# Optimization experiments

Hardware: AMD Instinct MI355X
Metric: run time of the kernel (lower is better)

The kernel has to match this reference:

```python
import jax, jax.numpy as jnp
import numpy as np

NUM_NODES = 10000
NODE_DIM = 128
EDGE_DIM = 128
HIDDEN_DIM = 128
OUT_DIM = 128
N_EDGES = 640000


def setup_inputs() -> dict:
    key = jax.random.key(0)
    k = jax.random.split(key, 8)
    x = jax.random.normal(k[0], (NUM_NODES, NODE_DIM), dtype=jnp.float32)
    edge_index = jax.random.randint(k[1], (2, N_EDGES), 0, NUM_NODES, dtype=jnp.int64)
    edge_attr = jax.random.normal(k[2], (N_EDGES, EDGE_DIM), dtype=jnp.float32)
    # node2edge linear: in = 2*node_dim + edge_dim
    s1 = 1.0 / np.sqrt(2 * NODE_DIM + EDGE_DIM)
    W1 = jax.random.uniform(k[3], (2 * NODE_DIM + EDGE_DIM, HIDDEN_DIM), jnp.float32, -s1, s1)
    b1 = jax.random.uniform(k[4], (HIDDEN_DIM,), jnp.float32, -s1, s1)
    # edge2node linear: in = hidden_dim + node_dim
    s2 = 1.0 / np.sqrt(HIDDEN_DIM + NODE_DIM)
    W2 = jax.random.uniform(k[5], (HIDDEN_DIM + NODE_DIM, OUT_DIM), jnp.float32, -s2, s2)
    b2 = jax.random.uniform(k[6], (OUT_DIM,), jnp.float32, -s2, s2)
    return {"x": x, "edge_index": edge_index, "edge_attr": edge_attr,
            "W1": W1, "b1": b1, "W2": W2, "b2": b2}


def reference(x, edge_index, edge_attr, W1, b1, W2, b2):
    src, dst = edge_index[0], edge_index[1]
    # Node2Edge: gather endpoints, concat with edge features, linear
    h_i = x[src]                                   # [E, node_dim]
    h_j = x[dst]                                   # [E, node_dim]
    inp_e = jnp.concatenate([h_i, h_j, edge_attr], axis=-1)  # [E, 2*nd+ed]
    h_edge = inp_e @ W1 + b1                       # [E, hidden]
    # Edge2Node: scatter-sum edge embeddings to target nodes (edge_index[1])
    agg = jax.ops.segment_sum(h_edge, dst, num_segments=NUM_NODES)  # [N, hidden]
    inp_n = jnp.concatenate([agg, x], axis=-1)     # [N, hidden+nd]
    h_node = inp_n @ W2 + b2                       # [N, out]
    return h_node
```

## Files before the change

kernel.cpp:

```cpp
#include <hip/hip_runtime.h>


#define NN 10000
#define ED 640000
#define D  128

typedef __bf16 bf16;
typedef bf16  bf16x8 __attribute__((ext_vector_type(8)));
typedef float f32x4  __attribute__((ext_vector_type(4)));

__device__ __forceinline__ bf16 f2b(float f) {
  unsigned u = __builtin_bit_cast(unsigned, f);
  u += 0x7fffu + ((u >> 16) & 1u);
  unsigned short h = (unsigned short)(u >> 16);
  return __builtin_bit_cast(bf16, h);
}

__device__ __forceinline__ bf16x8 bzero8() {
  bf16 z = __builtin_bit_cast(bf16, (unsigned short)0);
  bf16x8 v = {z, z, z, z, z, z, z, z};
  return v;
}

__global__ __launch_bounds__(256) void k_prep(const float* __restrict__ x,
                                              const float* __restrict__ W1,
                                              const float* __restrict__ W2,
                                              bf16* __restrict__ xb,
                                              bf16* __restrict__ W1p,
                                              bf16* __restrict__ W2p,
                                              int* __restrict__ counts) {
  int id = blockIdx.x * 256 + threadIdx.x;
  if (id < 160000) {
    int i = id * 8;
    f32x4 a = *(const f32x4*)(x + i);
    f32x4 b = *(const f32x4*)(x + i + 4);
    bf16x8 h;
    h[0]=f2b(a[0]); h[1]=f2b(a[1]); h[2]=f2b(a[2]); h[3]=f2b(a[3]);
    h[4]=f2b(b[0]); h[5]=f2b(b[1]); h[6]=f2b(b[2]); h[7]=f2b(b[3]);
    *(bf16x8*)(xb + i) = h;
  } else if (id < 170000) {
    counts[id - 160000] = 0;
  } else if (id < 176144) {
    int o8 = id - 170000;
    int kb = o8 >> 9, rem = o8 & 511, t = rem >> 6, L = rem & 63;
    int col  = t * 16 + (L & 15);
    int row0 = kb * 32 + (L >> 4) * 8;
    bf16x8 h;
    #pragma unroll
    for (int j = 0; j < 8; j++) h[j] = f2b(W1[(row0 + j) * D + col]);
    *(bf16x8*)(W1p + o8 * 8) = h;
  } else if (id < 180240) {
    int o8 = id - 176144;
    int kb = o8 >> 9, rem = o8 & 511, t = rem >> 6, L = rem & 63;
    int col  = t * 16 + (L & 15);
    int row0 = kb * 32 + (L >> 4) * 8;
    bf16x8 h;
    #pragma unroll
    for (int j = 0; j < 8; j++) h[j] = f2b(W2[(row0 + j) * D + col]);
    *(bf16x8*)(W2p + o8 * 8) = h;
  }
}

__global__ __launch_bounds__(256) void k_hist(const int* __restrict__ dst,
                                              int* __restrict__ counts) {
  int e = blockIdx.x * 256 + threadIdx.x;
  if (e < ED) atomicAdd(&counts[dst[e]], 1);
}

__global__ __launch_bounds__(256) void k_scan(const int* __restrict__ counts,
                                              int* __restrict__ row_ptr,
                                              int* __restrict__ fill_ptr) {
  __shared__ int part[256];
  int tid = threadIdx.x;
  const int CH = 40;
  int base = tid * CH;
  int sum = 0;
  for (int i = 0; i < CH; i++) { int idx = base + i; if (idx < NN) sum += counts[idx]; }
  part[tid] = sum;
  __syncthreads();
  for (int off = 1; off < 256; off <<= 1) {
    int v = (tid >= off) ? part[tid - off] : 0;
    __syncthreads();
    part[tid] += v;
    __syncthreads();
  }
  int run = part[tid] - sum;
  for (int i = 0; i < CH; i++) {
    int idx = base + i;
    if (idx < NN) { row_ptr[idx] = run; fill_ptr[idx] = run; run += counts[idx]; }
  }
  if (tid == 255) row_ptr[NN] = part[255];
}

__global__ __launch_bounds__(256) void k_fill(const int* __restrict__ src,
                                              const int* __restrict__ dst,
                                              int* __restrict__ fill_ptr,
                                              int2* __restrict__ csr) {
  int e = blockIdx.x * 256 + threadIdx.x;
  if (e < ED) {
    int d = dst[e];
    int pos = atomicAdd(&fill_ptr[d], 1);
    csr[pos] = make_int2(e, src[e]);
  }
}

__global__ __launch_bounds__(256) void k_sum(const bf16*  __restrict__ xb,
                                             const float* __restrict__ ea,
                                             const int*   __restrict__ row_ptr,
                                             const int2*  __restrict__ csr,
                                             float* __restrict__ sx,
                                             float* __restrict__ sea) {
  int gwave = (blockIdx.x * 256 + threadIdx.x) >> 6;
  if (gwave >= NN) return;
  int lane = threadIdx.x & 63;
  int g = lane >> 4, l = lane & 15;
  int e0 = row_ptr[gwave], e1 = row_ptr[gwave + 1];

  f32x4 ax0 = {0.f,0.f,0.f,0.f}, ax1 = {0.f,0.f,0.f,0.f};
  f32x4 ae0 = {0.f,0.f,0.f,0.f}, ae1 = {0.f,0.f,0.f,0.f};

  #pragma unroll 2
  for (int e = e0 + g; e < e1; e += 4) {
    int2 es = csr[e];
    bf16x8 hx = *(const bf16x8*)(xb + (size_t)es.y * D + l * 8);
    const float* ep = ea + (size_t)es.x * D + l * 8;
    f32x4 f0 = *(const f32x4*)ep;
    f32x4 f1 = *(const f32x4*)(ep + 4);
    ax0[0] += (float)hx[0]; ax0[1] += (float)hx[1];
    ax0[2] += (float)hx[2]; ax0[3] += (float)hx[3];
    ax1[0] += (float)hx[4]; ax1[1] += (float)hx[5];
    ax1[2] += (float)hx[6]; ax1[3] += (float)hx[7];
    ae0 += f0;
    ae1 += f1;
  }
  #pragma unroll
  for (int i = 0; i < 4; i++) {
    ax0[i] += __shfl_xor(ax0[i], 16, 64); ax0[i] += __shfl_xor(ax0[i], 32, 64);
    ax1[i] += __shfl_xor(ax1[i], 16, 64); ax1[i] += __shfl_xor(ax1[i], 32, 64);
    ae0[i] += __shfl_xor(ae0[i], 16, 64); ae0[i] += __shfl_xor(ae0[i], 32, 64);
    ae1[i] += __shfl_xor(ae1[i], 16, 64); ae1[i] += __shfl_xor(ae1[i], 32, 64);
  }
  if (lane < 16) {
    float* px = sx  + (size_t)gwave * D + l * 8;
    float* pe = sea + (size_t)gwave * D + l * 8;
    *(f32x4*)px       = ax0;
    *(f32x4*)(px + 4) = ax1;
    *(f32x4*)pe       = ae0;
    *(f32x4*)(pe + 4) = ae1;
  }
}

__global__ __launch_bounds__(256) void k_out(const float* __restrict__ sx,
                                             const float* __restrict__ sea,
                                             const bf16*  __restrict__ xb,
                                             const bf16*  __restrict__ W1p,
                                             const bf16*  __restrict__ W2p,
                                             const float* __restrict__ b1,
                                             const float* __restrict__ b2,
                                             const int*   __restrict__ row_ptr,
                                             float* __restrict__ out) {
  __shared__ __align__(16) bf16 lds[64 * 392];
  int tid  = threadIdx.x;
  int wave = tid >> 6, lane = tid & 63, quad = lane >> 4, l16 = lane & 15;
  int n0 = blockIdx.x * 64;

  #pragma unroll
  for (int i = 0; i < 4; i++) {
    int m = (tid >> 4) + 16 * i;
    int v = n0 + m;
    int cl = tid & 15;
    float cntf = (v < NN) ? (float)(row_ptr[v + 1] - row_ptr[v]) : 0.f;
    #pragma unroll
    for (int j = 0; j < 3; j++) {
      int c = cl + 16 * j;
      bf16x8 h;
      if (v < NN) {
        if (j == 0) {
          const float* p = sx + (size_t)v * D + cl * 8;
          f32x4 f0 = *(const f32x4*)p, f1 = *(const f32x4*)(p + 4);
          h[0]=f2b(f0[0]); h[1]=f2b(f0[1]); h[2]=f2b(f0[2]); h[3]=f2b(f0[3]);
          h[4]=f2b(f1[0]); h[5]=f2b(f1[1]); h[6]=f2b(f1[2]); h[7]=f2b(f1[3]);
        } else if (j == 1) {
          bf16x8 hx = *(const bf16x8*)(xb + (size_t)v * D + cl * 8);
          #pragma unroll
          for (int k = 0; k < 8; k++) h[k] = f2b((float)hx[k] * cntf);
        } else {
          const float* p = sea + (size_t)v * D + cl * 8;
          f32x4 f0 = *(const f32x4*)p, f1 = *(const f32x4*)(p + 4);
          h[0]=f2b(f0[0]); h[1]=f2b(f0[1]); h[2]=f2b(f0[2]); h[3]=f2b(f0[3]);
          h[4]=f2b(f1[0]); h[5]=f2b(f1[1]); h[6]=f2b(f1[2]); h[7]=f2b(f1[3]);
        }
      } else h = bzero8();
      *(bf16x8*)&lds[m * 392 + c * 8] = h;
    }
  }
  __syncthreads();

  f32x4 acc[4][2];
  #pragma unroll
  for (int mt = 0; mt < 4; mt++)
    #pragma unroll
    for (int tt = 0; tt < 2; tt++) acc[mt][tt] = (f32x4){0.f, 0.f, 0.f, 0.f};

  #pragma unroll
  for (int kb = 0; kb < 12; kb++) {
    bf16x8 B0 = *(const bf16x8*)(W1p + ((kb * 8 + wave * 2 + 0) * 64 + lane) * 8);
    bf16x8 B1 = *(const bf16x8*)(W1p + ((kb * 8 + wave * 2 + 1) * 64 + lane) * 8);
    #pragma unroll
    for (int mt = 0; mt < 4; mt++) {
      bf16x8 a = *(const bf16x8*)&lds[(mt * 16 + l16) * 392 + kb * 32 + quad * 8];
      acc[mt][0] = __builtin_amdgcn_mfma_f32_16x16x32_bf16(a, B0, acc[mt][0], 0, 0, 0);
      acc[mt][1] = __builtin_amdgcn_mfma_f32_16x16x32_bf16(a, B1, acc[mt][1], 0, 0, 0);
    }
  }
  __syncthreads();

  #pragma unroll
  for (int tt = 0; tt < 2; tt++) {
    int col = wave * 32 + tt * 16 + l16;
    float bb = b1[col];
    #pragma unroll
    for (int mt = 0; mt < 4; mt++)
      #pragma unroll
      for (int r = 0; r < 4; r++) {
        int m = mt * 16 + quad * 4 + r;
        int v = n0 + m;
        float cntf = (v < NN) ? (float)(row_ptr[v + 1] - row_ptr[v]) : 0.f;
        lds[m * 264 + col] = f2b(acc[mt][tt][r] + cntf * bb);
      }
  }
  #pragma unroll
  for (int i = 0; i < 4; i++) {
    int m = (tid >> 4) + 16 * i;
    int c = tid & 15;
    int v = n0 + m;
    bf16x8 h = (v < NN) ? *(const bf16x8*)(xb + (size_t)v * D + c * 8) : bzero8();
    *(bf16x8*)&lds[m * 264 + 128 + c * 8] = h;
  }
  __syncthreads();

  f32x4 acc2[4][2];
  #pragma unroll
  for (int mt = 0; mt < 4; mt++)
    #pragma unroll
    for (int tt = 0; tt < 2; tt++) acc2[mt][tt] = (f32x4){0.f, 0.f, 0.f, 0.f};

  #pragma unroll
  for (int kb = 0; kb < 8; kb++) {
    bf16x8 B0 = *(const bf16x8*)(W2p + ((kb * 8 + wave * 2 + 0) * 64 + lane) * 8);
    bf16x8 B1 = *(const bf16x8*)(W2p + ((kb * 8 + wave * 2 + 1) * 64 + lane) * 8);
    #pragma unroll
    for (int mt = 0; mt < 4; mt++) {
      bf16x8 a = *(const bf16x8*)&lds[(mt * 16 + l16) * 264 + kb * 32 + quad * 8];
      acc2[mt][0] = __builtin_amdgcn_mfma_f32_16x16x32_bf16(a, B0, acc2[mt][0], 0, 0, 0);
      acc2[mt][1] = __builtin_amdgcn_mfma_f32_16x16x32_bf16(a, B1, acc2[mt][1], 0, 0, 0);
    }
  }

  #pragma unroll
  for (int tt = 0; tt < 2; tt++) {
    int col = wave * 32 + tt * 16 + l16;
    float bb = b2[col];
    #pragma unroll
    for (int mt = 0; mt < 4; mt++)
      #pragma unroll
      for (int r = 0; r < 4; r++) {
        int v = n0 + mt * 16 + quad * 4 + r;
        if (v < NN) out[(size_t)v * D + col] = acc2[mt][tt][r] + bb;
      }
  }
}

extern "C" void kernel_launch(void* const* d_in, const int* in_sizes, int n_in,
                              void* d_out, int out_size, void* d_ws, size_t ws_size,
                              hipStream_t stream) {
  const float* x  = (const float*)d_in[0];
  const int*   ei = (const int*)  d_in[1];
  const float* ea = (const float*)d_in[2];
  const float* W1 = (const float*)d_in[3];
  const float* b1 = (const float*)d_in[4];
  const float* W2 = (const float*)d_in[5];
  const float* b2 = (const float*)d_in[6];
  float* out = (float*)d_out;

  char* ws = (char*)d_ws;
  size_t off = 0;
  auto alloc = [&](size_t bytes) -> void* {
    void* p = ws + off;
    off += (bytes + 255) & ~(size_t)255;
    return p;
  };
  bf16*  xb      = (bf16*)alloc((size_t)NN * D * 2);
  bf16*  W1p     = (bf16*)alloc(49152 * 2);
  bf16*  W2p     = (bf16*)alloc(32768 * 2);
  float* sx      = (float*)alloc((size_t)NN * D * 4);
  float* sea     = (float*)alloc((size_t)NN * D * 4);
  int*   counts  = (int*)alloc(NN * 4);
  int*   row_ptr = (int*)alloc((NN + 1) * 4);
  int*   fill_ptr= (int*)alloc(NN * 4);
  int2*  csr     = (int2*)alloc((size_t)ED * 8);
  (void)ws_size; (void)in_sizes; (void)n_in; (void)out_size;

  const int* src = ei;
  const int* dst = ei + ED;

  k_prep<<<705, 256, 0, stream>>>(x, W1, W2, xb, W1p, W2p, counts);
  k_hist<<<(ED + 255) / 256, 256, 0, stream>>>(dst, counts);
  k_scan<<<1, 256, 0, stream>>>(counts, row_ptr, fill_ptr);
  k_fill<<<(ED + 255) / 256, 256, 0, stream>>>(src, dst, fill_ptr, csr);
  k_sum<<<2500, 256, 0, stream>>>(xb, ea, row_ptr, csr, sx, sea);
  k_out<<<157, 256, 0, stream>>>(sx, sea, xb, W1p, W2p, b1, b2, row_ptr, out);
}
```

Measured before the change: 583.5 us.

## Build CSR with per-block shared-memory histograms instead of global atomics

Replaces the global-atomic histogram and fill with a two-level scheme. Each of 64 blocks histograms its slice of edges in LDS, a column scan turns the per-block counts into offsets, and the fill pass ranks edges with LDS atomics. This removes contended global atomics on the destination counts and fill pointers. In exchange it adds a kernel launch, a 64x10000 int scratch array, and runs only 64 blocks over 10000 edges each, which may underuse the GPU. Edge order within a node may also differ from before.

```diff
diff --git a/kernel.cpp b/kernel.cpp
--- a/kernel.cpp
+++ b/kernel.cpp
@@ -4,6 +4,8 @@
 #define NN 10000
 #define ED 640000
 #define D  128
+#define NB 64
+#define EPB (ED / NB)
 
 typedef __bf16 bf16;
 typedef bf16  bf16x8 __attribute__((ext_vector_type(8)));
@@ -27,8 +29,7 @@
                                               const float* __restrict__ W2,
                                               bf16* __restrict__ xb,
                                               bf16* __restrict__ W1p,
-                                              bf16* __restrict__ W2p,
-                                              int* __restrict__ counts) {
+                                              bf16* __restrict__ W2p) {
   int id = blockIdx.x * 256 + threadIdx.x;
   if (id < 160000) {
     int i = id * 8;
@@ -38,10 +39,8 @@
     h[0]=f2b(a[0]); h[1]=f2b(a[1]); h[2]=f2b(a[2]); h[3]=f2b(a[3]);
     h[4]=f2b(b[0]); h[5]=f2b(b[1]); h[6]=f2b(b[2]); h[7]=f2b(b[3]);
     *(bf16x8*)(xb + i) = h;
-  } else if (id < 170000) {
-    counts[id - 160000] = 0;
-  } else if (id < 176144) {
-    int o8 = id - 170000;
+  } else if (id < 166144) {
+    int o8 = id - 160000;
     int kb = o8 >> 9, rem = o8 & 511, t = rem >> 6, L = rem & 63;
     int col  = t * 16 + (L & 15);
     int row0 = kb * 32 + (L >> 4) * 8;
@@ -49,8 +48,8 @@
     #pragma unroll
     for (int j = 0; j < 8; j++) h[j] = f2b(W1[(row0 + j) * D + col]);
     *(bf16x8*)(W1p + o8 * 8) = h;
-  } else if (id < 180240) {
-    int o8 = id - 176144;
+  } else if (id < 170240) {
+    int o8 = id - 166144;
     int kb = o8 >> 9, rem = o8 & 511, t = rem >> 6, L = rem & 63;
     int col  = t * 16 + (L & 15);
     int row0 = kb * 32 + (L >> 4) * 8;
@@ -62,14 +61,34 @@
 }
 
 __global__ __launch_bounds__(256) void k_hist(const int* __restrict__ dst,
-                                              int* __restrict__ counts) {
-  int e = blockIdx.x * 256 + threadIdx.x;
-  if (e < ED) atomicAdd(&counts[dst[e]], 1);
+                                              int* __restrict__ hist) {
+  __shared__ int h[NN];
+  int b = blockIdx.x, tid = threadIdx.x;
+  for (int i = tid; i < NN; i += 256) h[i] = 0;
+  __syncthreads();
+  int base = b * EPB;
+  for (int i = tid; i < EPB; i += 256) atomicAdd(&h[dst[base + i]], 1);
+  __syncthreads();
+  int* outp = hist + (size_t)b * NN;
+  for (int i = tid; i < NN; i += 256) outp[i] = h[i];
+}
+
+__global__ __launch_bounds__(256) void k_colscan(int* __restrict__ hist,
+                                                 int* __restrict__ counts) {
+  int v = blockIdx.x * 256 + threadIdx.x;
+  if (v >= NN) return;
+  int run = 0;
+  #pragma unroll
+  for (int b = 0; b < NB; b++) {
+    int t = hist[b * NN + v];
+    hist[b * NN + v] = run;
+    run += t;
+  }
+  counts[v] = run;
 }
 
 __global__ __launch_bounds__(256) void k_scan(const int* __restrict__ counts,
-                                              int* __restrict__ row_ptr,
-                                              int* __restrict__ fill_ptr) {
+                                              int* __restrict__ row_ptr) {
   __shared__ int part[256];
   int tid = threadIdx.x;
   const int CH = 40;
@@ -87,19 +106,27 @@
   int run = part[tid] - sum;
   for (int i = 0; i < CH; i++) {
     int idx = base + i;
-    if (idx < NN) { row_ptr[idx] = run; fill_ptr[idx] = run; run += counts[idx]; }
+    if (idx < NN) { row_ptr[idx] = run; run += counts[idx]; }
   }
   if (tid == 255) row_ptr[NN] = part[255];
 }
 
 __global__ __launch_bounds__(256) void k_fill(const int* __restrict__ src,
                                               const int* __restrict__ dst,
-                                              int* __restrict__ fill_ptr,
+                                              const int* __restrict__ row_ptr,
+                                              const int* __restrict__ hist,
                                               int2* __restrict__ csr) {
-  int e = blockIdx.x * 256 + threadIdx.x;
-  if (e < ED) {
+  __shared__ int rk[NN];
+  int b = blockIdx.x, tid = threadIdx.x;
+  for (int i = tid; i < NN; i += 256) rk[i] = 0;
+  __syncthreads();
+  int base = b * EPB;
+  const int* __restrict__ hb = hist + (size_t)b * NN;
+  for (int i = tid; i < EPB; i += 256) {
+    int e = base + i;
     int d = dst[e];
-    int pos = atomicAdd(&fill_ptr[d], 1);
+    int r = atomicAdd(&rk[d], 1);
+    int pos = row_ptr[d] + hb[d] + r;
     csr[pos] = make_int2(e, src[e]);
   }
 }
@@ -297,17 +324,18 @@
   float* sea     = (float*)alloc((size_t)NN * D * 4);
   int*   counts  = (int*)alloc(NN * 4);
   int*   row_ptr = (int*)alloc((NN + 1) * 4);
-  int*   fill_ptr= (int*)alloc(NN * 4);
+  int*   hist    = (int*)alloc((size_t)NB * NN * 4);
   int2*  csr     = (int2*)alloc((size_t)ED * 8);
   (void)ws_size; (void)in_sizes; (void)n_in; (void)out_size;
 
   const int* src = ei;
   const int* dst = ei + ED;
 
-  k_prep<<<705, 256, 0, stream>>>(x, W1, W2, xb, W1p, W2p, counts);
-  k_hist<<<(ED + 255) / 256, 256, 0, stream>>>(dst, counts);
-  k_scan<<<1, 256, 0, stream>>>(counts, row_ptr, fill_ptr);
-  k_fill<<<(ED + 255) / 256, 256, 0, stream>>>(src, dst, fill_ptr, csr);
+  k_prep<<<665, 256, 0, stream>>>(x, W1, W2, xb, W1p, W2p);
+  k_hist<<<NB, 256, 0, stream>>>(dst, hist);
+  k_colscan<<<40, 256, 0, stream>>>(hist, counts);
+  k_scan<<<1, 256, 0, stream>>>(counts, row_ptr);
+  k_fill<<<NB, 256, 0, stream>>>(src, dst, row_ptr, hist, csr);
   k_sum<<<2500, 256, 0, stream>>>(xb, ea, row_ptr, csr, sx, sea);
   k_out<<<157, 256, 0, stream>>>(sx, sea, xb, W1p, W2p, b1, b2, row_ptr, out);
 }
```

Measured after the change: 567.6 us. -2.7%, faster.
